# Optimization experiments

Measured on AMD Instinct MI355X. Metric: run time of the kernel, lower is better.

## Reference

```python
import jax, jax.numpy as jnp
import numpy as np

K = 16  # top-k patches kept (module default)

def setup_inputs() -> dict:
    key = jax.random.key(0)
    ks = jax.random.split(key, 5)
    N, D, A, H = 100000, 1024, 128, 256
    x = jax.random.normal(ks[0], (N, D), dtype=jnp.float32)
    Wa1 = jax.random.normal(ks[1], (D, A), dtype=jnp.float32) * (1.0 / np.sqrt(D))
    ba1 = jnp.zeros((A,), dtype=jnp.float32)
    Wa2 = jax.random.normal(ks[2], (A, 1), dtype=jnp.float32) * (1.0 / np.sqrt(A))
    ba2 = jnp.zeros((1,), dtype=jnp.float32)
    Wc1 = jax.random.normal(ks[3], (D, H), dtype=jnp.float32) * (1.0 / np.sqrt(D))
    bc1 = jnp.zeros((H,), dtype=jnp.float32)
    Wc2 = jax.random.normal(ks[4], (H, 1), dtype=jnp.float32) * (1.0 / np.sqrt(H))
    bc2 = jnp.zeros((1,), dtype=jnp.float32)
    return {"x": x, "Wa1": Wa1, "ba1": ba1, "Wa2": Wa2, "ba2": ba2,
            "Wc1": Wc1, "bc1": bc1, "Wc2": Wc2, "bc2": bc2}

def reference(x, Wa1, ba1, Wa2, ba2, Wc1, bc1, Wc2, bc2):
    # attention logits: Linear -> tanh -> Linear, shape [N]
    scores = (jnp.tanh(x @ Wa1 + ba1) @ Wa2 + ba2)[:, 0]
    # top-k selection over patch dim (k < N here)
    top_vals, top_idx = jax.lax.top_k(scores, K)       # [K], [K]
    x_k = x[top_idx]                                    # [K, D] gather
    attn_w = jax.nn.softmax(top_vals)                   # renormalise over k
    slide_embedding = attn_w @ x_k                      # [D] weighted sum
    # classifier MLP (dropout is identity in eval)
    h = jax.nn.relu(slide_embedding @ Wc1 + bc1)
    logit = (h @ Wc2 + bc2)[0]
    # scatter attention weights back into full-length vector
    full_weights = jnp.zeros(x.shape[0], dtype=x.dtype).at[top_idx].set(attn_w)
    return logit, slide_embedding, full_weights, top_idx
```

## Files before the change

### kernel.cpp

```cpp
#include <hip/hip_runtime.h>
#include <cstddef>
#include <cstdint>

#define N_PATCH 100000
#define D_IN    1024
#define A_DIM   128
#define H_DIM   256
#define KTOP    16

#define OUT_LOGIT 0
#define OUT_EMB   1
#define OUT_FW    (1 + D_IN)
#define OUT_TOPI  (OUT_FW + N_PATCH)

#define WS_SCORES 0
#define WS_CANDV  (N_PATCH)
#define WS_CANDI  (N_PATCH + 4096)
#define WS_EMB    (N_PATCH + 2 * 4096)
#define WS_HPART  (WS_EMB + D_IN)
#define WS_WPK    (WS_HPART + 16 * H_DIM)

#define NB2A  256
#define CHUNK 391

typedef __attribute__((ext_vector_type(8))) short bf8_t;
typedef __attribute__((ext_vector_type(4))) float f4_t;

__global__ __launch_bounds__(256) void k_prepack(
    const float* __restrict__ Wa1, uint4* __restrict__ wpk)
{
    int t = blockIdx.x * 256 + threadIdx.x;
    int lane = t & 63;
    int nt   = (t >> 6) & 7;
    int ks   = t >> 9;
    int n  = nt * 16 + (lane & 15);
    int k0 = ks * 32 + ((lane >> 4) * 8);
    union { ushort u[8]; uint4 v; } o;
    #pragma unroll
    for (int j = 0; j < 8; ++j) {
        uint b = __float_as_uint(Wa1[(size_t)(k0 + j) * A_DIM + n]);
        o.u[j] = (ushort)((b + 0x7fffu + ((b >> 16) & 1u)) >> 16);
    }
    wpk[t] = o.v;
}

__device__ __forceinline__ void cvt8(const float4& a, const float4& b, bf8_t& out)
{
    union { uint u[4]; bf8_t v; } O;
    asm("v_cvt_pk_bf16_f32 %0, %1, %2" : "=v"(O.u[0]) : "v"(a.x), "v"(a.y));
    asm("v_cvt_pk_bf16_f32 %0, %1, %2" : "=v"(O.u[1]) : "v"(a.z), "v"(a.w));
    asm("v_cvt_pk_bf16_f32 %0, %1, %2" : "=v"(O.u[2]) : "v"(b.x), "v"(b.y));
    asm("v_cvt_pk_bf16_f32 %0, %1, %2" : "=v"(O.u[3]) : "v"(b.z), "v"(b.w));
    out = O.v;
}

#define MFMA_BF16 __builtin_amdgcn_mfma_f32_16x16x32_bf16

#define BAR_LDS() do {                                          \
    asm volatile("s_waitcnt lgkmcnt(0)" ::: "memory");          \
    __builtin_amdgcn_s_barrier();                               \
    asm volatile("" ::: "memory");                              \
} while (0)

#define SCORE_STEP(IT, PAR, CUR) do {                                          \
    bf8_t ah0, ah1;                                                            \
    cvt8(A##CUR[0], A##CUR[1], ah0);                                           \
    cvt8(A##CUR[2], A##CUR[3], ah1);                                           \
    if ((PAR) == 0) {                                                          \
        _Pragma("unroll")                                                      \
        for (int i = 0; i < 4; ++i) sB[bufp ^ 1][tid + i * 256] = bpre[i];     \
        const int vtp = (t0 + (IT) + 2) & 15;                                  \
        _Pragma("unroll")                                                      \
        for (int i = 0; i < 4; ++i) bpre[i] = wpk[vtp * 1024 + tid + i * 256]; \
    }                                                                          \
    {                                                                          \
        const int kg2 = (((t0 + (IT) + 1) & 15) * 2 + (PAR)) * 32;             \
        A##CUR[0] = *(const float4*)(pa0 + kg2);                               \
        A##CUR[1] = *(const float4*)(pa0 + kg2 + 4);                           \
        A##CUR[2] = *(const float4*)(pa1 + kg2);                               \
        A##CUR[3] = *(const float4*)(pa1 + kg2 + 4);                           \
    }                                                                          \
    const bf8_t* sBf = (const bf8_t*)sB[bufp] + (PAR) * 512;                   \
    _Pragma("unroll")                                                          \
    for (int nt = 0; nt < 8; nt += 2) {                                        \
        bf8_t b0 = sBf[nt * 64 + ln];                                          \
        bf8_t b1 = sBf[(nt + 1) * 64 + ln];                                    \
        acc[0][nt]     = MFMA_BF16(ah0, b0, acc[0][nt],     0, 0, 0);          \
        acc[1][nt]     = MFMA_BF16(ah1, b0, acc[1][nt],     0, 0, 0);          \
        acc[0][nt + 1] = MFMA_BF16(ah0, b1, acc[0][nt + 1], 0, 0, 0);          \
        acc[1][nt + 1] = MFMA_BF16(ah1, b1, acc[1][nt + 1], 0, 0, 0);          \
    }                                                                          \
    if (PAR) BAR_LDS();                                                        \
} while (0)

__global__ __launch_bounds__(256) void k_scores(
    const float* __restrict__ x, const uint4* __restrict__ wpk,
    const float* __restrict__ ba1, const float* __restrict__ Wa2,
    const float* __restrict__ ba2, float* __restrict__ scores)
{
    __shared__ uint4 sB[2][1024];

    const int tid = threadIdx.x;
    const int ln  = tid & 63;
    const int q   = ln >> 4;
    const int c   = ln & 15;
    const int wv  = tid >> 6;
    const int row0 = blockIdx.x * 128 + wv * 32;
    const int t0   = blockIdx.x & 15;

    const int r0 = min(row0 + c,      N_PATCH - 1);
    const int r1 = min(row0 + 16 + c, N_PATCH - 1);
    const float* pa0 = x + (size_t)r0 * D_IN + q * 8;
    const float* pa1 = x + (size_t)r1 * D_IN + q * 8;

    f4_t acc[2][8];
    #pragma unroll
    for (int rt = 0; rt < 2; ++rt)
        #pragma unroll
        for (int nt = 0; nt < 8; ++nt)
            acc[rt][nt] = (f4_t){0.f, 0.f, 0.f, 0.f};

    uint4 bpre[4];
    {
        uint4 b0[4];
        #pragma unroll
        for (int i = 0; i < 4; ++i) b0[i] = wpk[t0 * 1024 + tid + i * 256];
        #pragma unroll
        for (int i = 0; i < 4; ++i) sB[0][tid + i * 256] = b0[i];
    }
    {
        const int t1 = (t0 + 1) & 15;
        #pragma unroll
        for (int i = 0; i < 4; ++i) bpre[i] = wpk[t1 * 1024 + tid + i * 256];
    }

    float4 A0[4], A1[4];
    {
        const int ka = (t0 * 2) * 32;
        const int kb = (t0 * 2 + 1) * 32;
        A0[0] = *(const float4*)(pa0 + ka);
        A0[1] = *(const float4*)(pa0 + ka + 4);
        A0[2] = *(const float4*)(pa1 + ka);
        A0[3] = *(const float4*)(pa1 + ka + 4);
        A1[0] = *(const float4*)(pa0 + kb);
        A1[1] = *(const float4*)(pa0 + kb + 4);
        A1[2] = *(const float4*)(pa1 + kb);
        A1[3] = *(const float4*)(pa1 + kb + 4);
    }

    BAR_LDS();

    for (int it = 0; it < 16; ++it) {
        const int bufp = it & 1;
        SCORE_STEP(it, 0, 0);
        SCORE_STEP(it, 1, 1);
    }

    float b1v[8], w2v[8];
    #pragma unroll
    for (int nt = 0; nt < 8; ++nt) {
        b1v[nt] = ba1[nt * 16 + c];
        w2v[nt] = Wa2[nt * 16 + c];
    }
    const float b2 = ba2[0];

    #pragma unroll
    for (int rt = 0; rt < 2; ++rt)
        #pragma unroll
        for (int reg = 0; reg < 4; ++reg) {
            float p = 0.f;
            #pragma unroll
            for (int nt = 0; nt < 8; ++nt)
                p += tanhf(acc[rt][nt][reg] + b1v[nt]) * w2v[nt];
            #pragma unroll
            for (int off = 1; off < 16; off <<= 1)
                p += __shfl_xor(p, off, 64);
            if (c == 0) {
                int row = row0 + rt * 16 + q * 4 + reg;
                if (row < N_PATCH) scores[row] = p + b2;
            }
        }
}

__global__ __launch_bounds__(256) void k_topk_local(
    const float* __restrict__ scores, float* __restrict__ candv,
    int* __restrict__ candi, float* __restrict__ out_fw)
{
    __shared__ float sv[512];
    __shared__ float rv[256];
    __shared__ int   rs[256];
    const int tid  = threadIdx.x;
    const int base = blockIdx.x * CHUNK;

    for (int i = tid; i < 512; i += 256) {
        int g = base + i;
        sv[i] = (i < CHUNK && g < N_PATCH) ? scores[g] : -1e30f;
    }
    for (int i = tid; i < CHUNK; i += 256) {
        int g = base + i;
        if (g < N_PATCH) out_fw[g] = 0.f;
    }
    __syncthreads();

    for (int r = 0; r < KTOP; ++r) {
        float v1 = sv[tid], v2 = sv[tid + 256];
        float bv; int bs;
        if (v2 > v1) { bv = v2; bs = tid + 256; } else { bv = v1; bs = tid; }
        rv[tid] = bv; rs[tid] = bs;
        __syncthreads();
        for (int off = 128; off > 0; off >>= 1) {
            if (tid < off) {
                float ov = rv[tid + off]; int os = rs[tid + off];
                if (ov > rv[tid] || (ov == rv[tid] && os < rs[tid])) {
                    rv[tid] = ov; rs[tid] = os;
                }
            }
            __syncthreads();
        }
        if (tid == 0) {
            int s = rs[0];
            candv[blockIdx.x * KTOP + r] = rv[0];
            candi[blockIdx.x * KTOP + r] = base + s;
            sv[s] = -1e30f;
        }
        __syncthreads();
    }
}

__global__ __launch_bounds__(256) void k_finalize(
    const float* __restrict__ candv, const int* __restrict__ candi,
    const float* __restrict__ x, const float* __restrict__ Wa1,
    const float* __restrict__ ba1, const float* __restrict__ Wa2,
    const float* __restrict__ ba2, float* __restrict__ out,
    float* __restrict__ emb)
{
    __shared__ float cv[4096];
    __shared__ int   ci[4096];
    __shared__ float rv[256];
    __shared__ int   rgx[256];
    __shared__ int   rsl[256];
    __shared__ int   topi[KTOP];
    __shared__ float sxs[KTOP][D_IN] __attribute__((aligned(16)));
    __shared__ float sred[KTOP][128];
    __shared__ float exv[KTOP];
    __shared__ float attn[KTOP];
    __shared__ int   order[KTOP];
    const int tid = threadIdx.x;

    for (int i = tid; i < 4096; i += 256) { cv[i] = candv[i]; ci[i] = candi[i]; }
    __syncthreads();

    for (int r = 0; r < KTOP; ++r) {
        float bv = -1e38f; int bg = 0x7fffffff; int bs = tid * 16;
        #pragma unroll
        for (int i = 0; i < 16; ++i) {
            int s = tid * 16 + i;
            float v = cv[s]; int g = ci[s];
            if (v > bv || (v == bv && g < bg)) { bv = v; bg = g; bs = s; }
        }
        rv[tid] = bv; rgx[tid] = bg; rsl[tid] = bs;
        __syncthreads();
        for (int off = 128; off > 0; off >>= 1) {
            if (tid < off) {
                if (rv[tid + off] > rv[tid] ||
                    (rv[tid + off] == rv[tid] && rgx[tid + off] < rgx[tid])) {
                    rv[tid] = rv[tid + off]; rgx[tid] = rgx[tid + off]; rsl[tid] = rsl[tid + off];
                }
            }
            __syncthreads();
        }
        if (tid == 0) {
            topi[r] = rgx[0]; cv[rsl[0]] = -1e30f;
        }
        __syncthreads();
    }

    for (int r = 0; r < KTOP; ++r)
        for (int d = tid; d < D_IN; d += 256)
            sxs[r][d] = x[(size_t)topi[r] * D_IN + d];
    __syncthreads();

    {
        const int g = tid >> 7, n = tid & 127;
        float ac[8];
        #pragma unroll
        for (int rr = 0; rr < 8; ++rr) ac[rr] = 0.f;
        #pragma unroll 4
        for (int d = 0; d < D_IN; ++d) {
            const float w = Wa1[(size_t)d * A_DIM + n];
            #pragma unroll
            for (int rr = 0; rr < 8; ++rr)
                ac[rr] = fmaf(sxs[g * 8 + rr][d], w, ac[rr]);
        }
        const float bn = ba1[n], wn = Wa2[n];
        #pragma unroll
        for (int rr = 0; rr < 8; ++rr)
            sred[g * 8 + rr][n] = tanhf(ac[rr] + bn) * wn;
    }
    __syncthreads();
    if (tid < KTOP) {
        float s = ba2[0];
        for (int n = 0; n < 128; ++n) s += sred[tid][n];
        exv[tid] = s;
    }
    __syncthreads();

    if (tid == 0) {
        #pragma unroll
        for (int k2 = 0; k2 < KTOP; ++k2) order[k2] = k2;
        for (int a2 = 1; a2 < KTOP; ++a2)
            for (int b2 = a2; b2 > 0; --b2) {
                int i1 = order[b2 - 1], i2 = order[b2];
                bool sw = (exv[i2] > exv[i1]) ||
                          (exv[i2] == exv[i1] && topi[i2] < topi[i1]);
                if (sw) { order[b2 - 1] = i2; order[b2] = i1; } else break;
            }
        float mx = exv[order[0]];
        float ssum = 0.f;
        for (int k2 = 0; k2 < KTOP; ++k2) {
            float e = expf(exv[order[k2]] - mx);
            attn[k2] = e; ssum += e;
        }
        float inv = 1.f / ssum;
        for (int k2 = 0; k2 < KTOP; ++k2) attn[k2] *= inv;
    }
    __syncthreads();

    if (tid < KTOP) {
        int src = order[tid];
        out[OUT_TOPI + tid] = (float)topi[src];
        out[OUT_FW + topi[src]] = attn[tid];
    }

    float4 e = {0.f, 0.f, 0.f, 0.f};
    #pragma unroll
    for (int k2 = 0; k2 < KTOP; ++k2) {
        const int src = order[k2];
        const float a = attn[k2];
        const float4 xv = *(const float4*)(&sxs[src][tid * 4]);
        e.x = fmaf(a, xv.x, e.x);
        e.y = fmaf(a, xv.y, e.y);
        e.z = fmaf(a, xv.z, e.z);
        e.w = fmaf(a, xv.w, e.w);
    }
    out[OUT_EMB + tid * 4 + 0] = e.x;
    out[OUT_EMB + tid * 4 + 1] = e.y;
    out[OUT_EMB + tid * 4 + 2] = e.z;
    out[OUT_EMB + tid * 4 + 3] = e.w;
    *(float4*)(emb + tid * 4) = e;
}

__global__ __launch_bounds__(256) void k_mlp1(
    const float* __restrict__ emb, const float* __restrict__ Wc1,
    float* __restrict__ hpart)
{
    __shared__ float se[64];
    const int b = blockIdx.x, tid = threadIdx.x;
    if (tid < 64) se[tid] = emb[b * 64 + tid];
    __syncthreads();
    float p = 0.f;
    #pragma unroll 8
    for (int d = 0; d < 64; ++d)
        p = fmaf(se[d], Wc1[(size_t)(b * 64 + d) * H_DIM + tid], p);
    hpart[b * H_DIM + tid] = p;
}

__global__ __launch_bounds__(256) void k_logit(
    const float* __restrict__ hpart, const float* __restrict__ bc1,
    const float* __restrict__ Wc2, const float* __restrict__ bc2,
    float* __restrict__ out)
{
    __shared__ float red[256];
    const int tid = threadIdx.x;
    float h = bc1[tid];
    #pragma unroll
    for (int i = 0; i < 16; ++i) h += hpart[i * H_DIM + tid];
    h = fmaxf(h, 0.f) * Wc2[tid];
    red[tid] = h;
    __syncthreads();
    for (int off = 128; off > 0; off >>= 1) {
        if (tid < off) red[tid] += red[tid + off];
        __syncthreads();
    }
    if (tid == 0) out[OUT_LOGIT] = red[0] + bc2[0];
}

extern "C" void kernel_launch(void* const* d_in, const int* in_sizes, int n_in,
                              void* d_out, int out_size, void* d_ws, size_t ws_size,
                              hipStream_t stream)
{
    const float* x   = (const float*)d_in[0];
    const float* Wa1 = (const float*)d_in[1];
    const float* ba1 = (const float*)d_in[2];
    const float* Wa2 = (const float*)d_in[3];
    const float* ba2 = (const float*)d_in[4];
    const float* Wc1 = (const float*)d_in[5];
    const float* bc1 = (const float*)d_in[6];
    const float* Wc2 = (const float*)d_in[7];
    const float* bc2 = (const float*)d_in[8];
    float* out = (float*)d_out;
    float* ws  = (float*)d_ws;

    float* scores = ws + WS_SCORES;
    float* candv  = ws + WS_CANDV;
    int*   candi  = (int*)(ws + WS_CANDI);
    float* emb    = ws + WS_EMB;
    float* hpart  = ws + WS_HPART;
    uint4* wpk    = (uint4*)(ws + WS_WPK);

    dim3 blk(256);
    k_prepack<<<64, blk, 0, stream>>>(Wa1, wpk);
    k_scores<<<(N_PATCH + 127) / 128, blk, 0, stream>>>(x, wpk, ba1, Wa2, ba2, scores);
    k_topk_local<<<NB2A, blk, 0, stream>>>(scores, candv, candi, out + OUT_FW);
    k_finalize<<<1, blk, 0, stream>>>(candv, candi, x, Wa1, ba1, Wa2, ba2, out, emb);
    k_mlp1<<<16, blk, 0, stream>>>(emb, Wc1, hpart);
    k_logit<<<1, blk, 0, stream>>>(hpart, bc1, Wc2, bc2, out);
}
```

Before: 830.0 us.

## Split single-block finalize into select, parallel rescore, and final kernels; deepen A prefetch

The single-block finalize kernel used to gather the 16 winning rows and run a full 1024x128 fp32 rescore matvec on one CU. That work is now split: one block selects the top-k, 16 blocks each rescore a 64-wide slice of D and write partial sums, and a final single block reduces the partials, applies tanh, runs the softmax and builds the embedding straight from global x. Separately, the score kernel now double-buffers its A-row register loads across two iterations, so prefetch distance goes from one step to two. The cost is more register pressure, two extra kernel launches and a round trip of partial sums through global memory.

```diff
diff --git a/kernel.cpp b/kernel.cpp
--- a/kernel.cpp
+++ b/kernel.cpp
@@ -16,9 +16,11 @@
 #define WS_SCORES 0
 #define WS_CANDV  (N_PATCH)
 #define WS_CANDI  (N_PATCH + 4096)
-#define WS_EMB    (N_PATCH + 2 * 4096)
+#define WS_TOPI   (N_PATCH + 2 * 4096)
+#define WS_EMB    (WS_TOPI + 16)
 #define WS_HPART  (WS_EMB + D_IN)
-#define WS_WPK    (WS_HPART + 16 * H_DIM)
+#define WS_HP2    (WS_HPART + 16 * H_DIM)
+#define WS_WPK    (WS_HP2 + 16 * KTOP * 128)
 
 #define NB2A  256
 #define CHUNK 391
@@ -62,25 +64,27 @@
     asm volatile("" ::: "memory");                              \
 } while (0)
 
-#define SCORE_STEP(IT, PAR, CUR) do {                                          \
+#define LOADA(BUF, IT, PAR) do {                                               \
+    const int kg = (((t0 + (IT)) & 15) * 2 + (PAR)) * 32;                      \
+    A##BUF[0] = *(const float4*)(pa0 + kg);                                    \
+    A##BUF[1] = *(const float4*)(pa0 + kg + 4);                                \
+    A##BUF[2] = *(const float4*)(pa1 + kg);                                    \
+    A##BUF[3] = *(const float4*)(pa1 + kg + 4);                                \
+} while (0)
+
+#define SCORE_STEP(IT, PAR, BUF, BUFP) do {                                    \
     bf8_t ah0, ah1;                                                            \
-    cvt8(A##CUR[0], A##CUR[1], ah0);                                           \
-    cvt8(A##CUR[2], A##CUR[3], ah1);                                           \
+    cvt8(A##BUF[0], A##BUF[1], ah0);                                           \
+    cvt8(A##BUF[2], A##BUF[3], ah1);                                           \
     if ((PAR) == 0) {                                                          \
         _Pragma("unroll")                                                      \
-        for (int i = 0; i < 4; ++i) sB[bufp ^ 1][tid + i * 256] = bpre[i];     \
+        for (int i = 0; i < 4; ++i) sB[(BUFP) ^ 1][tid + i * 256] = bpre[i];   \
         const int vtp = (t0 + (IT) + 2) & 15;                                  \
         _Pragma("unroll")                                                      \
         for (int i = 0; i < 4; ++i) bpre[i] = wpk[vtp * 1024 + tid + i * 256]; \
     }                                                                          \
-    {                                                                          \
-        const int kg2 = (((t0 + (IT) + 1) & 15) * 2 + (PAR)) * 32;             \
-        A##CUR[0] = *(const float4*)(pa0 + kg2);                               \
-        A##CUR[1] = *(const float4*)(pa0 + kg2 + 4);                           \
-        A##CUR[2] = *(const float4*)(pa1 + kg2);                               \
-        A##CUR[3] = *(const float4*)(pa1 + kg2 + 4);                           \
-    }                                                                          \
-    const bf8_t* sBf = (const bf8_t*)sB[bufp] + (PAR) * 512;                   \
+    LOADA(BUF, (IT) + 2, PAR);                                                 \
+    const bf8_t* sBf = (const bf8_t*)sB[BUFP] + (PAR) * 512;                   \
     _Pragma("unroll")                                                          \
     for (int nt = 0; nt < 8; nt += 2) {                                        \
         bf8_t b0 = sBf[nt * 64 + ln];                                          \
@@ -134,26 +138,19 @@
         for (int i = 0; i < 4; ++i) bpre[i] = wpk[t1 * 1024 + tid + i * 256];
     }
 
-    float4 A0[4], A1[4];
-    {
-        const int ka = (t0 * 2) * 32;
-        const int kb = (t0 * 2 + 1) * 32;
-        A0[0] = *(const float4*)(pa0 + ka);
-        A0[1] = *(const float4*)(pa0 + ka + 4);
-        A0[2] = *(const float4*)(pa1 + ka);
-        A0[3] = *(const float4*)(pa1 + ka + 4);
-        A1[0] = *(const float4*)(pa0 + kb);
-        A1[1] = *(const float4*)(pa0 + kb + 4);
-        A1[2] = *(const float4*)(pa1 + kb);
-        A1[3] = *(const float4*)(pa1 + kb + 4);
-    }
+    float4 AE0[4], AE1[4], AO0[4], AO1[4];
+    LOADA(E0, 0, 0);
+    LOADA(E1, 0, 1);
+    LOADA(O0, 1, 0);
+    LOADA(O1, 1, 1);
 
     BAR_LDS();
 
-    for (int it = 0; it < 16; ++it) {
-        const int bufp = it & 1;
-        SCORE_STEP(it, 0, 0);
-        SCORE_STEP(it, 1, 1);
+    for (int it = 0; it < 16; it += 2) {
+        SCORE_STEP(it,     0, E0, 0);
+        SCORE_STEP(it,     1, E1, 0);
+        SCORE_STEP(it + 1, 0, O0, 1);
+        SCORE_STEP(it + 1, 1, O1, 1);
     }
 
     float b1v[8], w2v[8];
@@ -227,24 +224,15 @@
     }
 }
 
-__global__ __launch_bounds__(256) void k_finalize(
+__global__ __launch_bounds__(256) void k_select(
     const float* __restrict__ candv, const int* __restrict__ candi,
-    const float* __restrict__ x, const float* __restrict__ Wa1,
-    const float* __restrict__ ba1, const float* __restrict__ Wa2,
-    const float* __restrict__ ba2, float* __restrict__ out,
-    float* __restrict__ emb)
+    int* __restrict__ topi_ws)
 {
     __shared__ float cv[4096];
     __shared__ int   ci[4096];
     __shared__ float rv[256];
     __shared__ int   rgx[256];
     __shared__ int   rsl[256];
-    __shared__ int   topi[KTOP];
-    __shared__ float sxs[KTOP][D_IN] __attribute__((aligned(16)));
-    __shared__ float sred[KTOP][128];
-    __shared__ float exv[KTOP];
-    __shared__ float attn[KTOP];
-    __shared__ int   order[KTOP];
     const int tid = threadIdx.x;
 
     for (int i = tid; i < 4096; i += 256) { cv[i] = candv[i]; ci[i] = candi[i]; }
@@ -270,32 +258,69 @@
             __syncthreads();
         }
         if (tid == 0) {
-            topi[r] = rgx[0]; cv[rsl[0]] = -1e30f;
+            topi_ws[r] = rgx[0]; cv[rsl[0]] = -1e30f;
         }
         __syncthreads();
     }
-
-    for (int r = 0; r < KTOP; ++r)
-        for (int d = tid; d < D_IN; d += 256)
-            sxs[r][d] = x[(size_t)topi[r] * D_IN + d];
-    __syncthreads();
+}
+
+__global__ __launch_bounds__(256) void k_rescore(
+    const float* __restrict__ x, const float* __restrict__ Wa1,
+    const int* __restrict__ topi_ws, float* __restrict__ hp)
+{
+    __shared__ float sx[KTOP][64];
+    __shared__ int   sti[KTOP];
+    const int b = blockIdx.x, tid = threadIdx.x;
+    if (tid < KTOP) sti[tid] = topi_ws[tid];
+    __syncthreads();
+    for (int i = tid; i < KTOP * 64; i += 256) {
+        int r = i >> 6, d = i & 63;
+        sx[r][d] = x[(size_t)sti[r] * D_IN + b * 64 + d];
+    }
+    __syncthreads();
+
+    const int n = tid & 127, h = tid >> 7;
+    float ac[8];
+    #pragma unroll
+    for (int rr = 0; rr < 8; ++rr) ac[rr] = 0.f;
+    #pragma unroll 4
+    for (int d = 0; d < 64; ++d) {
+        const float w = Wa1[(size_t)(b * 64 + d) * A_DIM + n];
+        #pragma unroll
+        for (int rr = 0; rr < 8; ++rr)
+            ac[rr] = fmaf(sx[h * 8 + rr][d], w, ac[rr]);
+    }
+    #pragma unroll
+    for (int rr = 0; rr < 8; ++rr)
+        hp[((size_t)b * KTOP + h * 8 + rr) * 128 + n] = ac[rr];
+}
+
+__global__ __launch_bounds__(256) void k_final2(
+    const float* __restrict__ hp, const float* __restrict__ ba1,
+    const float* __restrict__ Wa2, const float* __restrict__ ba2,
+    const float* __restrict__ x, const int* __restrict__ topi_ws,
+    float* __restrict__ out, float* __restrict__ emb)
+{
+    __shared__ float sred[KTOP][128];
+    __shared__ int   topi[KTOP];
+    __shared__ float exv[KTOP];
+    __shared__ float attn[KTOP];
+    __shared__ int   order[KTOP];
+    const int tid = threadIdx.x;
+    if (tid < KTOP) topi[tid] = topi_ws[tid];
 
     {
-        const int g = tid >> 7, n = tid & 127;
-        float ac[8];
-        #pragma unroll
-        for (int rr = 0; rr < 8; ++rr) ac[rr] = 0.f;
-        #pragma unroll 4
-        for (int d = 0; d < D_IN; ++d) {
-            const float w = Wa1[(size_t)d * A_DIM + n];
+        const int n = tid & 127, h = tid >> 7;
+        const float bn = ba1[n], wn = Wa2[n];
+        #pragma unroll
+        for (int rr = 0; rr < 8; ++rr) {
+            const int r = h * 8 + rr;
+            float s = 0.f;
             #pragma unroll
-            for (int rr = 0; rr < 8; ++rr)
-                ac[rr] = fmaf(sxs[g * 8 + rr][d], w, ac[rr]);
-        }
-        const float bn = ba1[n], wn = Wa2[n];
-        #pragma unroll
-        for (int rr = 0; rr < 8; ++rr)
-            sred[g * 8 + rr][n] = tanhf(ac[rr] + bn) * wn;
+            for (int b = 0; b < 16; ++b)
+                s += hp[((size_t)b * KTOP + r) * 128 + n];
+            sred[r][n] = tanhf(s + bn) * wn;
+        }
     }
     __syncthreads();
     if (tid < KTOP) {
@@ -337,7 +362,7 @@
     for (int k2 = 0; k2 < KTOP; ++k2) {
         const int src = order[k2];
         const float a = attn[k2];
-        const float4 xv = *(const float4*)(&sxs[src][tid * 4]);
+        const float4 xv = *(const float4*)(x + (size_t)topi[src] * D_IN + tid * 4);
         e.x = fmaf(a, xv.x, e.x);
         e.y = fmaf(a, xv.y, e.y);
         e.z = fmaf(a, xv.z, e.z);
@@ -404,15 +429,19 @@
     float* scores = ws + WS_SCORES;
     float* candv  = ws + WS_CANDV;
     int*   candi  = (int*)(ws + WS_CANDI);
+    int*   topi   = (int*)(ws + WS_TOPI);
     float* emb    = ws + WS_EMB;
     float* hpart  = ws + WS_HPART;
+    float* hp2    = ws + WS_HP2;
     uint4* wpk    = (uint4*)(ws + WS_WPK);
 
     dim3 blk(256);
     k_prepack<<<64, blk, 0, stream>>>(Wa1, wpk);
     k_scores<<<(N_PATCH + 127) / 128, blk, 0, stream>>>(x, wpk, ba1, Wa2, ba2, scores);
     k_topk_local<<<NB2A, blk, 0, stream>>>(scores, candv, candi, out + OUT_FW);
-    k_finalize<<<1, blk, 0, stream>>>(candv, candi, x, Wa1, ba1, Wa2, ba2, out, emb);
+    k_select<<<1, blk, 0, stream>>>(candv, candi, topi);
+    k_rescore<<<16, blk, 0, stream>>>(x, Wa1, topi, hp2);
+    k_final2<<<1, blk, 0, stream>>>(hp2, ba1, Wa2, ba2, x, topi, out, emb);
     k_mlp1<<<16, blk, 0, stream>>>(emb, Wc1, hpart);
     k_logit<<<1, blk, 0, stream>>>(hpart, bc1, Wc2, bc2, out);
 }
```

Measured after the change: 704.3 us. -15.1%, faster.
